# Optimization experiments

Hardware: AMD Instinct MI355X
Metric: run time of the kernel (lower is better)

The kernel has to match this reference:

```python
import jax, jax.numpy as jnp
import numpy as np

H = 16          # num_attention_heads
DH = 64         # attention_head_size
HID = H * DH    # hidden_size = 1024
EPS = 1e-12


def _layernorm(x, gamma, beta):
    mu = jnp.mean(x, axis=-1, keepdims=True)
    var = jnp.mean(jnp.square(x - mu), axis=-1, keepdims=True)
    return (x - mu) * jax.lax.rsqrt(var + EPS) * gamma + beta


def _attention(q, k, v, mask, Wo, bo, gamma, beta):
    # q,k,v: [B,S,HID] already linearly projected
    B, Tq, _ = q.shape
    Tk = k.shape[1]
    qh = q.reshape(B, Tq, H, DH)
    kh = k.reshape(B, Tk, H, DH)
    vh = v.reshape(B, Tk, H, DH)
    scores = jnp.einsum('bqhd,bkhd->bhqk', qh, kh) / np.sqrt(DH).astype(q.dtype)
    if mask is not None:
        scores = scores + mask  # mask broadcasts [B,1,1,Tk]
    probs = jax.nn.softmax(scores, axis=-1)
    ctx = jnp.einsum('bhqk,bkhd->bqhd', probs, vh)
    proj = jnp.einsum('bqhd,hdo->bqo', ctx, Wo) + bo
    # NOTE: residual is the projected query q (faithful to the source)
    return _layernorm(q + proj, gamma, beta)


def setup_inputs() -> dict:
    key = jax.random.key(0)
    ks = jax.random.split(key, 20)
    B, T, S = 4, 1024, 1024
    s = 0.02
    inp = {
        'encoder_states': jax.random.normal(ks[0], (B, S, HID), jnp.float32),
        'decoder_inputs': jax.random.normal(ks[1], (B, T, HID), jnp.float32),
        'src_attention_mask': jnp.zeros((B, 1, 1, S), jnp.float32),
        'tgt_attention_mask': jnp.zeros((B, 1, 1, T), jnp.float32),
        'Wq': jax.random.normal(ks[2], (HID, HID), jnp.float32) * s,
        'bq': jnp.zeros((HID,), jnp.float32),
        'Wk': jax.random.normal(ks[3], (HID, HID), jnp.float32) * s,
        'bk': jnp.zeros((HID,), jnp.float32),
        'Wv': jax.random.normal(ks[4], (HID, HID), jnp.float32) * s,
        'bv': jnp.zeros((HID,), jnp.float32),
        'Wq2': jax.random.normal(ks[5], (HID, HID), jnp.float32) * s,
        'bq2': jnp.zeros((HID,), jnp.float32),
        'Wk2': jax.random.normal(ks[6], (HID, HID), jnp.float32) * s,
        'bk2': jnp.zeros((HID,), jnp.float32),
        'Wv2': jax.random.normal(ks[7], (HID, HID), jnp.float32) * s,
        'bv2': jnp.zeros((HID,), jnp.float32),
        'Wo': jax.random.normal(ks[8], (H, DH, HID), jnp.float32) * s,
        'bo': jnp.zeros((HID,), jnp.float32),
        'gamma': jnp.ones((HID,), jnp.float32),
        'beta': jnp.zeros((HID,), jnp.float32),
    }
    return inp


def reference(encoder_states, decoder_inputs, src_attention_mask, tgt_attention_mask,
              Wq, bq, Wk, bk, Wv, bv, Wq2, bq2, Wk2, bk2, Wv2, bv2,
              Wo, bo, gamma, beta):
    # self-attention over decoder inputs
    q1 = decoder_inputs @ Wq + bq
    k1 = decoder_inputs @ Wk + bk
    v1 = decoder_inputs @ Wv + bv
    self_out = _attention(q1, k1, v1, tgt_attention_mask, Wo, bo, gamma, beta)
    # cross-attention: query from self_out, key/value from encoder states
    q2 = self_out @ Wq2 + bq2
    k2 = encoder_states @ Wk2 + bk2
    v2 = encoder_states @ Wv2 + bv2
    return _attention(q2, k2, v2, src_attention_mask, Wo, bo, gamma, beta)
```

## Files before the change

kernel.cpp:

```cpp
#include <hip/hip_runtime.h>
#include <stdint.h>


typedef unsigned short u16;
typedef __bf16 bf16x8 __attribute__((ext_vector_type(8)));
typedef float f32x4 __attribute__((ext_vector_type(4)));

#define AS1 __attribute__((address_space(1)))
#define AS3 __attribute__((address_space(3)))

#define VMCNT(n) asm volatile("s_waitcnt vmcnt(" #n ")" ::: "memory")
#define SBARRIER() asm volatile("s_barrier" ::: "memory")

__device__ __forceinline__ u16 f2bf(float f) {
  union { float f; uint32_t u; } v; v.f = f;
  uint32_t u = v.u;
  return (u16)((u + 0x7fffu + ((u >> 16) & 1u)) >> 16);
}

__device__ __forceinline__ uint32_t cvt_pk_bf16(float lo, float hi) {
  uint32_t r;
  asm("v_cvt_pk_bf16_f32 %0, %1, %2" : "=v"(r) : "v"(lo), "v"(hi));
  return r;
}

__device__ __forceinline__ void gl_lds16(const void* g, void* l) {
  __builtin_amdgcn_global_load_lds((AS1 void*)(g), (AS3 void*)(l), 16, 0, 0);
}

__device__ __forceinline__ int swz(int row, int byte) {
  return row * 128 + (byte ^ ((row & 7) << 4));
}

__global__ void __launch_bounds__(256)
convert2_kernel(const float* __restrict__ in0, u16* __restrict__ out0,
                const float* __restrict__ in1, u16* __restrict__ out1) {
  const int half = blockIdx.x >> 12;
  const int i = (blockIdx.x & 4095) * 256 + threadIdx.x;
  const float* in = half ? in1 : in0;
  u16* out = half ? out1 : out0;
  float4 v = ((const float4*)in)[i];
  ushort4 o;
  o.x = f2bf(v.x); o.y = f2bf(v.y); o.z = f2bf(v.z); o.w = f2bf(v.w);
  ((ushort4*)out)[i] = o;
}

struct WP { const float* w[7]; };

__global__ void __launch_bounds__(256)
transpose_kernel(WP wp, u16* __restrict__ out) {
  __shared__ float tile[64][65];
  const float* W = wp.w[blockIdx.z];
  u16* Wt = out + (size_t)blockIdx.z * 1024 * 1024;
  const int k0 = blockIdx.y * 64, n0 = blockIdx.x * 64;
  const int t = threadIdx.x;
  const int r = t >> 4, c4 = (t & 15) * 4;
#pragma unroll
  for (int rr = 0; rr < 64; rr += 16) {
    float4 v = *(const float4*)&W[(size_t)(k0 + r + rr) * 1024 + n0 + c4];
    tile[r + rr][c4 + 0] = v.x; tile[r + rr][c4 + 1] = v.y;
    tile[r + rr][c4 + 2] = v.z; tile[r + rr][c4 + 3] = v.w;
  }
  __syncthreads();
  const int n = t >> 2, seg = (t & 3) * 16;
  union { u16 s[16]; uint4 q[2]; } u;
#pragma unroll
  for (int i = 0; i < 16; ++i) u.s[i] = f2bf(tile[seg + i][n]);
  uint4* dst = (uint4*)&Wt[(size_t)(n0 + n) * 1024 + k0 + seg];
  dst[0] = u.q[0]; dst[1] = u.q[1];
}

__global__ void __launch_bounds__(512, 2)
qkv256_kernel(const u16* __restrict__ A0, const u16* __restrict__ A1,
              const u16* __restrict__ A2, const u16* __restrict__ Bt,
              const float* __restrict__ b0, const float* __restrict__ b1,
              const float* __restrict__ b2,
              u16* __restrict__ qb, float* __restrict__ qf,
              u16* __restrict__ kb, u16* __restrict__ vt) {
  __shared__ u16 Alds[2][256 * 32];
  __shared__ u16 Blds[2][256 * 32];
  const int bm = blockIdx.y * 256, bn = blockIdx.x * 256;
  const int seg = bn >> 10;
  const u16* A = (seg == 0) ? A0 : (seg == 1) ? A1 : A2;
  const int t = threadIdx.x, wv = t >> 6, ln = t & 63;
  const int wm = (wv >> 2) * 128, wn = (wv & 3) * 64;
  const int lcol = ln & 15, lk8 = (ln >> 4) * 8, lr4 = (ln >> 4) * 4;

  f32x4 acc[8][4] = {};

  auto STAGE = [&](int buf, int k0) {
#pragma unroll
    for (int c = 0; c < 2; ++c) {
      const int o = c * 8192 + wv * 1024 + ln * 16;
      const int row = o >> 6, colb = o & 63;
      gl_lds16((const char*)A + ((size_t)(bm + row) * 1024 + k0) * 2 + colb,
               (char*)Alds[buf] + c * 8192 + wv * 1024);
      gl_lds16((const char*)Bt + ((size_t)(bn + row) * 1024 + k0) * 2 + colb,
               (char*)Blds[buf] + c * 8192 + wv * 1024);
    }
  };

  auto COMPUTE = [&](int buf) {
    const u16* Ab = Alds[buf];
    const u16* Bb = Blds[buf];
    bf16x8 a[8], b[4];
#pragma unroll
    for (int j = 0; j < 4; ++j)
      b[j] = *(const bf16x8*)&Bb[(wn + j * 16 + lcol) * 32 + lk8];
#pragma unroll
    for (int i = 0; i < 8; ++i)
      a[i] = *(const bf16x8*)&Ab[(wm + i * 16 + lcol) * 32 + lk8];
#pragma unroll
    for (int i = 0; i < 8; ++i)
#pragma unroll
      for (int j = 0; j < 4; ++j)
        acc[i][j] = __builtin_amdgcn_mfma_f32_16x16x32_bf16(a[i], b[j], acc[i][j], 0, 0, 0);
  };

  STAGE(0, 0);
  int cur = 0;
  for (int it = 0; it < 31; ++it) {
    STAGE(cur ^ 1, (it + 1) * 32);
    VMCNT(4);
    SBARRIER();
    COMPUTE(cur);
    SBARRIER();
    cur ^= 1;
  }
  VMCNT(0);
  SBARRIER();
  COMPUTE(cur);

  const int cs = bn & 1023;
  const float* bias = (seg == 0) ? b0 : (seg == 1) ? b1 : b2;
#pragma unroll
  for (int j = 0; j < 4; ++j) {
    const int col = cs + wn + j * 16 + lcol;
    const float bc = bias[col];
#pragma unroll
    for (int i = 0; i < 8; ++i) {
      const int row0 = bm + wm + i * 16 + lr4;
      if (seg == 2) {
        ushort4 o;
        o.x = f2bf(acc[i][j][0] + bc); o.y = f2bf(acc[i][j][1] + bc);
        o.z = f2bf(acc[i][j][2] + bc); o.w = f2bf(acc[i][j][3] + bc);
        const int b_ = row0 >> 10, s = row0 & 1023;
        const int h = col >> 6, d = col & 63;
        *(ushort4*)&vt[(((size_t)(b_ * 16 + h) * 64 + d) << 10) + s] = o;
      } else if (seg == 0) {
#pragma unroll
        for (int r = 0; r < 4; ++r) {
          const size_t idx = (size_t)(row0 + r) * 1024 + col;
          const float v = acc[i][j][r] + bc;
          qb[idx] = f2bf(v); qf[idx] = v;
        }
      } else {
#pragma unroll
        for (int r = 0; r < 4; ++r) {
          const size_t idx = (size_t)(row0 + r) * 1024 + col;
          kb[idx] = f2bf(acc[i][j][r] + bc);
        }
      }
    }
  }
}

__global__ void __launch_bounds__(256)
gemm_proj(const u16* __restrict__ A, const u16* __restrict__ Bt,
          const float* __restrict__ bias, const float* __restrict__ resid,
          float* __restrict__ outf) {
  __shared__ u16 Alds[2][8192];
  __shared__ u16 Blds[2][8192];
  const int bm = blockIdx.y * 128, bn = blockIdx.x * 128;
  const int t = threadIdx.x, wv = t >> 6, ln = t & 63;
  const int wm = (wv >> 1) * 64, wn = (wv & 1) * 64;
  const int lcol = ln & 15, lk8 = (ln >> 4) * 8, lr4 = (ln >> 4) * 4;

  f32x4 acc[4][4] = {};

  auto STAGE = [&](int buf, int k0) {
#pragma unroll
    for (int c = 0; c < 4; ++c) {
      const int o = c * 4096 + wv * 1024 + ln * 16;
      const int row = o >> 7, colb = o & 127;
      gl_lds16((const char*)A + ((size_t)(bm + row) * 1024 + k0) * 2 + colb,
               (char*)Alds[buf] + c * 4096 + wv * 1024);
      gl_lds16((const char*)Bt + ((size_t)(bn + row) * 1024 + k0) * 2 + colb,
               (char*)Blds[buf] + c * 4096 + wv * 1024);
    }
  };

  auto COMPUTE = [&](int buf) {
    const u16* Ab = Alds[buf];
    const u16* Bb = Blds[buf];
#pragma unroll
    for (int ks = 0; ks < 2; ++ks) {
      bf16x8 a[4], b[4];
#pragma unroll
      for (int i = 0; i < 4; ++i)
        a[i] = *(const bf16x8*)&Ab[(wm + i * 16 + lcol) * 64 + ks * 32 + lk8];
#pragma unroll
      for (int j = 0; j < 4; ++j)
        b[j] = *(const bf16x8*)&Bb[(wn + j * 16 + lcol) * 64 + ks * 32 + lk8];
#pragma unroll
      for (int i = 0; i < 4; ++i)
#pragma unroll
        for (int j = 0; j < 4; ++j)
          acc[i][j] = __builtin_amdgcn_mfma_f32_16x16x32_bf16(a[i], b[j], acc[i][j], 0, 0, 0);
    }
  };

  STAGE(0, 0);
  int cur = 0;
  for (int it = 0; it < 15; ++it) {
    STAGE(cur ^ 1, (it + 1) * 64);
    VMCNT(8);
    SBARRIER();
    COMPUTE(cur);
    SBARRIER();
    cur ^= 1;
  }
  VMCNT(0);
  SBARRIER();
  COMPUTE(cur);

#pragma unroll
  for (int j = 0; j < 4; ++j) {
    const int col = bn + wn + j * 16 + lcol;
    const float bc = bias[col];
#pragma unroll
    for (int i = 0; i < 4; ++i) {
      const int row0 = bm + wm + i * 16 + lr4;
#pragma unroll
      for (int r = 0; r < 4; ++r) {
        const size_t idx = (size_t)(row0 + r) * 1024 + col;
        outf[idx] = acc[i][j][r] + bc + resid[idx];
      }
    }
  }
}

__global__ void __launch_bounds__(256)
attn_kernel(const u16* __restrict__ Q, const u16* __restrict__ Kb,
            const u16* __restrict__ Vt, const float* __restrict__ mask,
            u16* __restrict__ ctx) {
  __shared__ u16 Klds[2][64 * 64];
  __shared__ u16 Vlds[2][64 * 64];
  __shared__ u16 Plds[4][16 * 64];

  const int fid = blockIdx.x;
  const int xcd = fid & 7, idx = fid >> 3;
  const int bh = xcd * 8 + (idx >> 4);
  const int b = bh >> 4, h = bh & 15;
  const int q0 = (idx & 15) * 64;

  const int t = threadIdx.x, wv = t >> 6, ln = t & 63;
  const int lcol = ln & 15, g = ln >> 4;
  const int lk8 = g * 8, c0 = g * 16;

  const int qrow = q0 + wv * 16 + lcol;
  const u16* qptr = Q + ((size_t)(b * 1024 + qrow) * 1024 + h * 64);
  bf16x8 qa[2];
  qa[0] = *(const bf16x8*)(qptr + lk8);
  qa[1] = *(const bf16x8*)(qptr + 32 + lk8);

  const float* mrow = mask + b * 1024;
  char* pbase = (char*)&Plds[wv][0];

  f32x4 accO[4] = {};
  float m_r = -1e30f, l_r = 0.f;

  auto STAGE = [&](int buf, int s0) {
#pragma unroll
    for (int c = 0; c < 2; ++c) {
      const int o = c * 4096 + wv * 1024 + ln * 16;
      const int row = o >> 7;
      const int src_cb = (o & 127) ^ ((row & 7) << 4);
      gl_lds16((const char*)Kb + ((size_t)((b * 1024 + s0 + row) * 1024 + h * 64)) * 2 + src_cb,
               (char*)Klds[buf] + c * 4096 + wv * 1024);
      gl_lds16((const char*)Vt + ((size_t)(((b * 16 + h) * 64 + row) * 1024 + s0)) * 2 + src_cb,
               (char*)Vlds[buf] + c * 4096 + wv * 1024);
    }
  };

  auto TILE = [&](int buf, const float4* mk) {
    f32x4 accST[4] = {};
    __builtin_amdgcn_s_setprio(1);
#pragma unroll
    for (int ks = 0; ks < 2; ++ks)
#pragma unroll
      for (int sb = 0; sb < 4; ++sb) {
        bf16x8 kb = *(const bf16x8*)((const char*)Klds[buf] + swz(sb * 16 + lcol, ks * 64 + c0));
        accST[sb] = __builtin_amdgcn_mfma_f32_16x16x32_bf16(kb, qa[ks], accST[sb], 0, 0, 0);
      }
    __builtin_amdgcn_s_setprio(0);

    float sv[4][4];
#pragma unroll
    for (int sb = 0; sb < 4; ++sb) {
      sv[sb][0] = accST[sb][0] * 0.125f + mk[sb].x;
      sv[sb][1] = accST[sb][1] * 0.125f + mk[sb].y;
      sv[sb][2] = accST[sb][2] * 0.125f + mk[sb].z;
      sv[sb][3] = accST[sb][3] * 0.125f + mk[sb].w;
    }
    float mt = sv[0][0];
#pragma unroll
    for (int sb = 0; sb < 4; ++sb)
#pragma unroll
      for (int r = 0; r < 4; ++r) mt = fmaxf(mt, sv[sb][r]);
    mt = fmaxf(mt, __shfl_xor(mt, 16));
    mt = fmaxf(mt, __shfl_xor(mt, 32));

    const float mn = fmaxf(m_r, mt);
    const float alpha = __expf(m_r - mn);
    m_r = mn;
    float rs = 0.f;
#pragma unroll
    for (int sb = 0; sb < 4; ++sb)
#pragma unroll
      for (int r = 0; r < 4; ++r) {
        const float pp = __expf(sv[sb][r] - mn);
        sv[sb][r] = pp;
        rs += pp;
      }
    rs += __shfl_xor(rs, 16);
    rs += __shfl_xor(rs, 32);
    l_r = l_r * alpha + rs;

#pragma unroll
    for (int sb = 0; sb < 4; ++sb) {
      uint2 dd;
      dd.x = cvt_pk_bf16(sv[sb][0], sv[sb][1]);
      dd.y = cvt_pk_bf16(sv[sb][2], sv[sb][3]);
      *(uint2*)(pbase + swz(lcol, sb * 32 + g * 8)) = dd;
    }

#pragma unroll
    for (int df = 0; df < 4; ++df)
#pragma unroll
      for (int r = 0; r < 4; ++r) accO[df][r] *= alpha;
    __builtin_amdgcn_s_setprio(1);
#pragma unroll
    for (int ks = 0; ks < 2; ++ks) {
      bf16x8 pb = *(const bf16x8*)(pbase + swz(lcol, ks * 64 + c0));
#pragma unroll
      for (int df = 0; df < 4; ++df) {
        bf16x8 va = *(const bf16x8*)((const char*)Vlds[buf] + swz(df * 16 + lcol, ks * 64 + c0));
        accO[df] = __builtin_amdgcn_mfma_f32_16x16x32_bf16(va, pb, accO[df], 0, 0, 0);
      }
    }
    __builtin_amdgcn_s_setprio(0);
  };

  STAGE(0, 0);
  float4 mk_cur[4];
#pragma unroll
  for (int sb = 0; sb < 4; ++sb)
    mk_cur[sb] = *(const float4*)&mrow[sb * 16 + g * 4];

  int cur = 0;
  for (int ti = 0; ti < 15; ++ti) {
    const int s1 = ti * 64 + 64;
    STAGE(cur ^ 1, s1);
    float4 mk_nxt[4];
#pragma unroll
    for (int sb = 0; sb < 4; ++sb)
      mk_nxt[sb] = *(const float4*)&mrow[s1 + sb * 16 + g * 4];
    VMCNT(12);
    SBARRIER();
    TILE(cur, mk_cur);
    SBARRIER();
#pragma unroll
    for (int sb = 0; sb < 4; ++sb) mk_cur[sb] = mk_nxt[sb];
    cur ^= 1;
  }
  VMCNT(4);
  SBARRIER();
  TILE(cur, mk_cur);

  const float inv = 1.0f / l_r;
  u16* cp = ctx + ((size_t)(b * 1024 + qrow) * 1024 + h * 64);
#pragma unroll
  for (int df = 0; df < 4; ++df) {
    ushort4 o;
    o.x = f2bf(accO[df][0] * inv); o.y = f2bf(accO[df][1] * inv);
    o.z = f2bf(accO[df][2] * inv); o.w = f2bf(accO[df][3] * inv);
    *(ushort4*)(cp + df * 16 + g * 4) = o;
  }
}

template <int OUTF>
__global__ void __launch_bounds__(256)
ln_kernel(const float* __restrict__ x, const float* __restrict__ gamma,
          const float* __restrict__ beta, float* __restrict__ outf,
          u16* __restrict__ outb) {
  const int row = blockIdx.x, t = threadIdx.x;
  const float* xr = x + (size_t)row * 1024;
  float4 v = *(const float4*)&xr[t * 4];
  float s = v.x + v.y + v.z + v.w;
  float q = v.x * v.x + v.y * v.y + v.z * v.z + v.w * v.w;
#pragma unroll
  for (int off = 1; off < 64; off <<= 1) {
    s += __shfl_xor(s, off);
    q += __shfl_xor(q, off);
  }
  __shared__ float ws[4], wq[4];
  if ((t & 63) == 0) { ws[t >> 6] = s; wq[t >> 6] = q; }
  __syncthreads();
  s = ws[0] + ws[1] + ws[2] + ws[3];
  q = wq[0] + wq[1] + wq[2] + wq[3];
  const float mu = s * (1.0f / 1024.0f);
  float var = q * (1.0f / 1024.0f) - mu * mu;
  var = fmaxf(var, 0.0f);
  const float rstd = rsqrtf(var + 1e-12f);
  float4 g = *(const float4*)&gamma[t * 4];
  float4 be = *(const float4*)&beta[t * 4];
  float y0 = (v.x - mu) * rstd * g.x + be.x;
  float y1 = (v.y - mu) * rstd * g.y + be.y;
  float y2 = (v.z - mu) * rstd * g.z + be.z;
  float y3 = (v.w - mu) * rstd * g.w + be.w;
  if constexpr (OUTF) {
    float4 o; o.x = y0; o.y = y1; o.z = y2; o.w = y3;
    *(float4*)&outf[(size_t)row * 1024 + t * 4] = o;
  } else {
    ushort4 o; o.x = f2bf(y0); o.y = f2bf(y1); o.z = f2bf(y2); o.w = f2bf(y3);
    *(ushort4*)&outb[(size_t)row * 1024 + t * 4] = o;
  }
}

extern "C" void kernel_launch(void* const* d_in, const int* in_sizes, int n_in,
                              void* d_out, int out_size, void* d_ws, size_t ws_size,
                              hipStream_t stream) {
  const float* enc = (const float*)d_in[0];
  const float* dec = (const float*)d_in[1];
  const float* src_mask = (const float*)d_in[2];
  const float* tgt_mask = (const float*)d_in[3];
  const float* Wq  = (const float*)d_in[4];  const float* bq  = (const float*)d_in[5];
  const float* Wk  = (const float*)d_in[6];  const float* bk  = (const float*)d_in[7];
  const float* Wv  = (const float*)d_in[8];  const float* bv  = (const float*)d_in[9];
  const float* Wq2 = (const float*)d_in[10]; const float* bq2 = (const float*)d_in[11];
  const float* Wk2 = (const float*)d_in[12]; const float* bk2 = (const float*)d_in[13];
  const float* Wv2 = (const float*)d_in[14]; const float* bv2 = (const float*)d_in[15];
  const float* Wo  = (const float*)d_in[16]; const float* bo  = (const float*)d_in[17];
  const float* gamma = (const float*)d_in[18]; const float* beta = (const float*)d_in[19];
  float* out = (float*)d_out;

  char* p = (char*)d_ws;
  const size_t ABF = (size_t)4096 * 1024 * 2;
  const size_t AF  = (size_t)4096 * 1024 * 4;
  const size_t WBF = (size_t)1024 * 1024 * 2;
  u16* decbf = (u16*)p; p += ABF;
  u16* encbf = (u16*)p; p += ABF;
  u16* wt    = (u16*)p; p += 7 * WBF;
  u16* qbf   = (u16*)p; p += ABF;
  float* qf  = (float*)p; p += AF;
  u16* kbf   = (u16*)p; p += ABF;
  u16* vtb   = (u16*)p; p += ABF;
  u16* ctxb  = (u16*)p; p += ABF;
  float* tmpf = (float*)p; p += AF;
  u16* sobf  = decbf;

  u16* WoT  = wt + 6 * 1048576;

  dim3 b256(256);
  convert2_kernel<<<8192, b256, 0, stream>>>(dec, decbf, enc, encbf);
  WP wp;
  wp.w[0] = Wq; wp.w[1] = Wk; wp.w[2] = Wv; wp.w[3] = Wq2;
  wp.w[4] = Wk2; wp.w[5] = Wv2; wp.w[6] = Wo;
  transpose_kernel<<<dim3(16, 16, 7), b256, 0, stream>>>(wp, wt);

  qkv256_kernel<<<dim3(12, 16), 512, 0, stream>>>(
      decbf, decbf, decbf, wt, bq, bk, bv, qbf, qf, kbf, vtb);
  attn_kernel<<<1024, b256, 0, stream>>>(qbf, kbf, vtb, tgt_mask, ctxb);
  gemm_proj<<<dim3(8, 32), b256, 0, stream>>>(ctxb, WoT, bo, qf, tmpf);
  ln_kernel<0><<<4096, b256, 0, stream>>>(tmpf, gamma, beta, nullptr, sobf);
  qkv256_kernel<<<dim3(12, 16), 512, 0, stream>>>(
      sobf, encbf, encbf, wt + 3 * 1048576, bq2, bk2, bv2, qbf, qf, kbf, vtb);
  attn_kernel<<<1024, b256, 0, stream>>>(qbf, kbf, vtb, src_mask, ctxb);
  gemm_proj<<<dim3(8, 32), b256, 0, stream>>>(ctxb, WoT, bo, qf, tmpf);
  ln_kernel<1><<<4096, b256, 0, stream>>>(tmpf, gamma, beta, out, nullptr);
}
```

Baseline: 259.1 us.

## Restructure QKV GEMM into 8-phase pipelined loop with swizzled 64-wide K tiles

Rewrites the fused QKV projection GEMM main loop to use BK=64 tiles with XOR-swizzled LDS layout, splitting each tile into four MFMA sub-phases. Global-to-LDS loads for the next tile are interleaved between phases, with explicit barriers, lgkmcnt waits, sched_barrier and s_setprio around MFMA bursts. This aims to hide load latency, reduce LDS bank conflicts and halve the loop iteration count. LDS usage doubles (128KB per block), which may limit occupancy to one block per CU despite the launch bounds.

```diff
diff --git a/kernel.cpp b/kernel.cpp
--- a/kernel.cpp
+++ b/kernel.cpp
@@ -8,8 +8,11 @@
 
 #define AS1 __attribute__((address_space(1)))
 #define AS3 __attribute__((address_space(3)))
+typedef AS3 char lds_char;
+typedef AS3 unsigned short lds_u16;
 
 #define VMCNT(n) asm volatile("s_waitcnt vmcnt(" #n ")" ::: "memory")
+#define LGKM0() asm volatile("s_waitcnt lgkmcnt(0)" ::: "memory")
 #define SBARRIER() asm volatile("s_barrier" ::: "memory")
 
 __device__ __forceinline__ u16 f2bf(float f) {
@@ -26,6 +29,12 @@
 
 __device__ __forceinline__ void gl_lds16(const void* g, void* l) {
   __builtin_amdgcn_global_load_lds((AS1 void*)(g), (AS3 void*)(l), 16, 0, 0);
+}
+
+__device__ __forceinline__ bf16x8 dsr128(const lds_u16* p) {
+  bf16x8 r;
+  asm volatile("ds_read_b128 %0, %1" : "=v"(r) : "v"(p));
+  return r;
 }
 
 __device__ __forceinline__ int swz(int row, int byte) {
@@ -71,65 +80,133 @@
 }
 
 __global__ void __launch_bounds__(512, 2)
-qkv256_kernel(const u16* __restrict__ A0, const u16* __restrict__ A1,
-              const u16* __restrict__ A2, const u16* __restrict__ Bt,
-              const float* __restrict__ b0, const float* __restrict__ b1,
-              const float* __restrict__ b2,
-              u16* __restrict__ qb, float* __restrict__ qf,
-              u16* __restrict__ kb, u16* __restrict__ vt) {
-  __shared__ u16 Alds[2][256 * 32];
-  __shared__ u16 Blds[2][256 * 32];
+qkv8p_kernel(const u16* __restrict__ A0, const u16* __restrict__ A1,
+             const u16* __restrict__ A2, const u16* __restrict__ Bt,
+             const float* __restrict__ b0, const float* __restrict__ b1,
+             const float* __restrict__ b2,
+             u16* __restrict__ qb, float* __restrict__ qf,
+             u16* __restrict__ kb, u16* __restrict__ vt) {
+  __shared__ u16 Alds[2][256 * 64];
+  __shared__ u16 Blds[2][256 * 64];
   const int bm = blockIdx.y * 256, bn = blockIdx.x * 256;
   const int seg = bn >> 10;
   const u16* A = (seg == 0) ? A0 : (seg == 1) ? A1 : A2;
   const int t = threadIdx.x, wv = t >> 6, ln = t & 63;
   const int wm = (wv >> 2) * 128, wn = (wv & 3) * 64;
-  const int lcol = ln & 15, lk8 = (ln >> 4) * 8, lr4 = (ln >> 4) * 4;
+  const int lcol = ln & 15, g = ln >> 4, lr4 = g * 4;
+  const int xr = (lcol & 7) << 4;
+  const int aoff0 = (g * 16) ^ xr;
+  const int aoff1 = (64 + g * 16) ^ xr;
+  lds_char* ABase = (lds_char*)&Alds[0][0];
+  lds_char* BBase = (lds_char*)&Blds[0][0];
 
   f32x4 acc[8][4] = {};
 
-  auto STAGE = [&](int buf, int k0) {
-#pragma unroll
-    for (int c = 0; c < 2; ++c) {
-      const int o = c * 8192 + wv * 1024 + ln * 16;
-      const int row = o >> 6, colb = o & 63;
-      gl_lds16((const char*)A + ((size_t)(bm + row) * 1024 + k0) * 2 + colb,
-               (char*)Alds[buf] + c * 8192 + wv * 1024);
-      gl_lds16((const char*)Bt + ((size_t)(bn + row) * 1024 + k0) * 2 + colb,
-               (char*)Blds[buf] + c * 8192 + wv * 1024);
-    }
-  };
-
-  auto COMPUTE = [&](int buf) {
-    const u16* Ab = Alds[buf];
-    const u16* Bb = Blds[buf];
-    bf16x8 a[8], b[4];
+  auto stageB = [&](int buf, int h, int k0) {
+#pragma unroll
+    for (int rd = 0; rd < 2; ++rd) {
+      const int row = h * 128 + rd * 64 + (t >> 3);
+      const int src = ((t & 7) * 16) ^ (((t >> 3) & 7) << 4);
+      gl_lds16((const char*)Bt + ((size_t)(bn + row) * 1024 + k0) * 2 + src,
+               (char*)&Blds[0][0] + buf * 32768 + h * 16384 + rd * 8192 + wv * 1024);
+    }
+  };
+  auto stageA = [&](int buf, int p, int k0) {
+#pragma unroll
+    for (int qq = 0; qq < 2; ++qq) {
+      const int q = p + qq * 2;
+      const int row = q * 64 + (t >> 3);
+      const int src = ((t & 7) * 16) ^ (((t >> 3) & 7) << 4);
+      gl_lds16((const char*)A + ((size_t)(bm + row) * 1024 + k0) * 2 + src,
+               (char*)&Alds[0][0] + buf * 32768 + q * 8192 + wv * 1024);
+    }
+  };
+
+  auto run_tile = [&](int cur, int nxt, int knxt, bool do_stage, bool fin) {
+    lds_char* Ac = ABase + cur * 32768;
+    lds_char* Bc = BBase + cur * 32768;
+    bf16x8 bfr[4], afr[4];
 #pragma unroll
     for (int j = 0; j < 4; ++j)
-      b[j] = *(const bf16x8*)&Bb[(wn + j * 16 + lcol) * 32 + lk8];
-#pragma unroll
-    for (int i = 0; i < 8; ++i)
-      a[i] = *(const bf16x8*)&Ab[(wm + i * 16 + lcol) * 32 + lk8];
-#pragma unroll
-    for (int i = 0; i < 8; ++i)
+      bfr[j] = dsr128((const lds_u16*)(Bc + (wn + j * 16 + lcol) * 128 + aoff0));
+#pragma unroll
+    for (int i = 0; i < 4; ++i)
+      afr[i] = dsr128((const lds_u16*)(Ac + (wm + i * 16 + lcol) * 128 + aoff0));
+    if (do_stage) stageB(nxt, 0, knxt);
+    if (fin) VMCNT(0);
+    __builtin_amdgcn_s_barrier();
+    LGKM0();
+    __builtin_amdgcn_sched_barrier(0);
+    __builtin_amdgcn_s_setprio(1);
+#pragma unroll
+    for (int i = 0; i < 4; ++i)
 #pragma unroll
       for (int j = 0; j < 4; ++j)
-        acc[i][j] = __builtin_amdgcn_mfma_f32_16x16x32_bf16(a[i], b[j], acc[i][j], 0, 0, 0);
-  };
-
-  STAGE(0, 0);
-  int cur = 0;
-  for (int it = 0; it < 31; ++it) {
-    STAGE(cur ^ 1, (it + 1) * 32);
-    VMCNT(4);
-    SBARRIER();
-    COMPUTE(cur);
-    SBARRIER();
-    cur ^= 1;
-  }
-  VMCNT(0);
-  SBARRIER();
-  COMPUTE(cur);
+        acc[i][j] = __builtin_amdgcn_mfma_f32_16x16x32_bf16(afr[i], bfr[j], acc[i][j], 0, 0, 0);
+    __builtin_amdgcn_s_setprio(0);
+    if (!fin) VMCNT(2);
+    __builtin_amdgcn_s_barrier();
+#pragma unroll
+    for (int i = 0; i < 4; ++i)
+      afr[i] = dsr128((const lds_u16*)(Ac + (wm + 64 + i * 16 + lcol) * 128 + aoff0));
+    if (do_stage) stageB(nxt, 1, knxt);
+    __builtin_amdgcn_s_barrier();
+    LGKM0();
+    __builtin_amdgcn_sched_barrier(0);
+    __builtin_amdgcn_s_setprio(1);
+#pragma unroll
+    for (int i = 0; i < 4; ++i)
+#pragma unroll
+      for (int j = 0; j < 4; ++j)
+        acc[4 + i][j] = __builtin_amdgcn_mfma_f32_16x16x32_bf16(afr[i], bfr[j], acc[4 + i][j], 0, 0, 0);
+    __builtin_amdgcn_s_setprio(0);
+    __builtin_amdgcn_s_barrier();
+#pragma unroll
+    for (int j = 0; j < 4; ++j)
+      bfr[j] = dsr128((const lds_u16*)(Bc + (wn + j * 16 + lcol) * 128 + aoff1));
+#pragma unroll
+    for (int i = 0; i < 4; ++i)
+      afr[i] = dsr128((const lds_u16*)(Ac + (wm + i * 16 + lcol) * 128 + aoff1));
+    if (do_stage) stageA(nxt, 0, knxt);
+    __builtin_amdgcn_s_barrier();
+    LGKM0();
+    __builtin_amdgcn_sched_barrier(0);
+    __builtin_amdgcn_s_setprio(1);
+#pragma unroll
+    for (int i = 0; i < 4; ++i)
+#pragma unroll
+      for (int j = 0; j < 4; ++j)
+        acc[i][j] = __builtin_amdgcn_mfma_f32_16x16x32_bf16(afr[i], bfr[j], acc[i][j], 0, 0, 0);
+    __builtin_amdgcn_s_setprio(0);
+    __builtin_amdgcn_s_barrier();
+#pragma unroll
+    for (int i = 0; i < 4; ++i)
+      afr[i] = dsr128((const lds_u16*)(Ac + (wm + 64 + i * 16 + lcol) * 128 + aoff1));
+    if (do_stage) stageA(nxt, 1, knxt);
+    __builtin_amdgcn_s_barrier();
+    LGKM0();
+    __builtin_amdgcn_sched_barrier(0);
+    __builtin_amdgcn_s_setprio(1);
+#pragma unroll
+    for (int i = 0; i < 4; ++i)
+#pragma unroll
+      for (int j = 0; j < 4; ++j)
+        acc[4 + i][j] = __builtin_amdgcn_mfma_f32_16x16x32_bf16(afr[i], bfr[j], acc[4 + i][j], 0, 0, 0);
+    __builtin_amdgcn_s_setprio(0);
+    if (do_stage) VMCNT(2);
+    __builtin_amdgcn_s_barrier();
+  };
+
+  stageB(0, 0, 0); stageB(0, 1, 0); stageA(0, 0, 0); stageA(0, 1, 0);
+  VMCNT(2);
+  __builtin_amdgcn_s_barrier();
+
+  for (int kt = 0; kt < 14; kt += 2) {
+    run_tile(0, 1, (kt + 1) * 64, true, false);
+    run_tile(1, 0, (kt + 2) * 64, true, false);
+  }
+  run_tile(0, 1, 960, true, false);
+  run_tile(1, 0, 0, false, true);
 
   const int cs = bn & 1023;
   const float* bias = (seg == 0) ? b0 : (seg == 1) ? b1 : b2;
@@ -469,12 +546,12 @@
   wp.w[4] = Wk2; wp.w[5] = Wv2; wp.w[6] = Wo;
   transpose_kernel<<<dim3(16, 16, 7), b256, 0, stream>>>(wp, wt);
 
-  qkv256_kernel<<<dim3(12, 16), 512, 0, stream>>>(
+  qkv8p_kernel<<<dim3(12, 16), 512, 0, stream>>>(
       decbf, decbf, decbf, wt, bq, bk, bv, qbf, qf, kbf, vtb);
   attn_kernel<<<1024, b256, 0, stream>>>(qbf, kbf, vtb, tgt_mask, ctxb);
   gemm_proj<<<dim3(8, 32), b256, 0, stream>>>(ctxb, WoT, bo, qf, tmpf);
   ln_kernel<0><<<4096, b256, 0, stream>>>(tmpf, gamma, beta, nullptr, sobf);
-  qkv256_kernel<<<dim3(12, 16), 512, 0, stream>>>(
+  qkv8p_kernel<<<dim3(12, 16), 512, 0, stream>>>(
       sobf, encbf, encbf, wt + 3 * 1048576, bq2, bk2, bv2, qbf, qf, kbf, vtb);
   attn_kernel<<<1024, b256, 0, stream>>>(qbf, kbf, vtb, src_mask, ctxb);
   gemm_proj<<<dim3(8, 32), b256, 0, stream>>>(ctxb, WoT, bo, qf, tmpf);
```

Result: faster. 242.1 us (-6.5%).
